# Kernel optimization log

Measured on AMD Instinct MI355X. Metric: run time of the kernel, lower is better.

The kernel has to match this reference:

```python
import jax, jax.numpy as jnp
import numpy as np

B, S, E, H, C = 2, 2048, 1024, 16, 16
SQ2 = np.float32(np.sqrt(2.0))


def setup_inputs() -> dict:
    key = jax.random.key(0)
    ks = jax.random.split(key, 32)
    sc = 0.02
    d = {"query": jax.random.normal(ks[0], (B, S, E), jnp.float32)}
    i = 1
    for dom in ("f", "w", "c"):
        d[f"Wp_{dom}"] = jax.random.normal(ks[i], (E, E), jnp.float32) * sc; i += 1
        d[f"bp_{dom}"] = jnp.zeros((E,), jnp.float32)
        d[f"Wc_{dom}"] = jax.random.normal(ks[i], (C, E, 3), jnp.float32) * sc; i += 1
        d[f"bc_{dom}"] = jnp.zeros((C,), jnp.float32)
        d["F" + dom] = jax.random.normal(ks[i], (C, E), jnp.float32); i += 1
    d["mha_iw"] = jax.random.normal(ks[i], (3 * E, E), jnp.float32) * sc; i += 1
    d["mha_ib"] = jnp.zeros((3 * E,), jnp.float32)
    d["mha_ow"] = jax.random.normal(ks[i], (E, E), jnp.float32) * sc; i += 1
    d["mha_ob"] = jnp.zeros((E,), jnp.float32)
    d["fus_W"] = jax.random.normal(ks[i], (E, 3 * E), jnp.float32) * sc; i += 1
    d["fus_b"] = jnp.zeros((E,), jnp.float32)
    return d


def _conv1d(x, W, b):
    # x: [B,S,E] real -> [B,S,C], conv over sequence, kernel 3, same padding
    y = jax.lax.conv_general_dilated(x.transpose(0, 2, 1), W, (1,), [(1, 1)],
                                     dimension_numbers=("NCH", "OIH", "NCH"))
    return (y + b[None, :, None]).transpose(0, 2, 1)


def _channels(x, Wc, bc, Fp):
    # spectral conv (real/imag separately if complex) + adaptive softmax filtering
    if jnp.iscomplexobj(x):
        ch = _conv1d(x.real, Wc, bc) + 1j * _conv1d(x.imag, Wc, bc)
    else:
        ch = _conv1d(x, Wc, bc)
    fw = jax.nn.softmax(Fp, axis=0)  # [C,E], softmax over channels
    return jnp.einsum("bsc,ce->bse", ch, fw.astype(ch.dtype))


def _spec_attn(q, k, v):
    scale = np.float32(1.0) / jnp.sqrt(jnp.asarray(q.shape[-1], jnp.float32))
    scores = jnp.einsum("bse,bte->bst", q, k) * scale
    if jnp.iscomplexobj(scores):
        w = jax.nn.softmax(scores.real, axis=-1)
        cw = (w * jnp.exp(1j * jnp.angle(scores))).astype(jnp.complex64)
        return jnp.einsum("bst,bte->bse", cw, v)
    return jnp.einsum("bst,bte->bse", jax.nn.softmax(scores, axis=-1), v)


def _haar(x):
    # simplified Haar wavelet transform; S is a power of 2 so no padding needed
    cur, coeffs = x, []
    while cur.shape[1] > 1:
        e, o = cur[:, 0::2, :], cur[:, 1::2, :]
        coeffs.append((e - o) / SQ2)
        cur = (e + o) / SQ2
    coeffs.append(cur)
    return jnp.concatenate(coeffs[::-1], axis=1)


def _dct_mats(L):
    n = jnp.arange(L, dtype=jnp.float32)
    k = n[:, None]
    D = jnp.cos(np.pi * k * (2.0 * n + 1.0) / (2.0 * L))
    D = D.at[0].multiply(np.float32(np.sqrt(1.0 / L)))
    D = D.at[1:].multiply(np.float32(np.sqrt(2.0 / L)))
    I = jnp.cos(np.pi * n * (2.0 * k + 1.0) / (2.0 * L))
    I = I.at[:, 0].multiply(np.float32(np.sqrt(1.0 / L)))
    I = I.at[:, 1:].multiply(np.float32(np.sqrt(2.0 / L)))
    return D, I


def _domain(x, Wp, bp, Wc, bc, Fp, domain):
    # key=value=query so q_domain == k_domain == v_domain
    xd = x @ Wp.T + bp
    if domain == "fourier":
        s = jnp.fft.fft(xd, axis=1)
        ch = _channels(s, Wc, bc, Fp)
        out = _spec_attn(ch, ch, ch)
        return jnp.fft.ifft(out, axis=1).real
    elif domain == "wavelet":
        s = _haar(xd)
        ch = _channels(s, Wc, bc, Fp)
        return _spec_attn(ch, ch, ch)  # inverse wavelet is identity in source
    else:  # cosine
        D, I = _dct_mats(xd.shape[1])
        s = jnp.einsum("st,bte->bse", D, xd)
        ch = _channels(s, Wc, bc, Fp)
        out = _spec_attn(ch, ch, ch)
        return jnp.einsum("st,bte->bse", I, out)


def _mha(x, iw, ib, ow, ob, nheads):
    # torch nn.MultiheadAttention (batch_first) self-attention
    Bx, L, Ex = x.shape
    hd = Ex // nheads
    qkv = x @ iw.T + ib
    q, k, v = jnp.split(qkv, 3, axis=-1)
    sh = lambda t: t.reshape(Bx, L, nheads, hd).transpose(0, 2, 1, 3)
    q, k, v = sh(q), sh(k), sh(v)
    a = jax.nn.softmax(jnp.einsum("bhld,bhmd->bhlm", q, k) / np.float32(np.sqrt(hd)), axis=-1)
    o = jnp.einsum("bhlm,bhmd->bhld", a, v).transpose(0, 2, 1, 3).reshape(Bx, L, Ex)
    return o @ ow.T + ob


def reference(query, Wp_f, bp_f, Wc_f, bc_f, Ff, Wp_w, bp_w, Wc_w, bc_w, Fw,
              Wp_c, bp_c, Wc_c, bc_c, Fc, mha_iw, mha_ib, mha_ow, mha_ob, fus_W, fus_b):
    outs = [
        _domain(query, Wp_f, bp_f, Wc_f, bc_f, Ff, "fourier"),
        _domain(query, Wp_w, bp_w, Wc_w, bc_w, Fw, "wavelet"),
        _domain(query, Wp_c, bp_c, Wc_c, bc_c, Fc, "cosine"),
    ]
    Bq, Sq, Eq = query.shape
    stacked = jnp.stack(outs, axis=2)                 # [B,S,3,E]
    corr = _mha(stacked.reshape(Bq * Sq, 3, Eq), mha_iw, mha_ib, mha_ow, mha_ob, H)
    fused = corr.reshape(Bq, Sq, 3 * Eq)              # concat of correlated domain outputs
    return fused @ fus_W.T + fus_b
```

## Files before the change

kernel.cpp:

```cpp
#include <hip/hip_runtime.h>
#include <cmath>

#define BB 2
#define SS_ 2048
#define EE 1024
#define CC 16

typedef __attribute__((ext_vector_type(8))) short short8v;
typedef __attribute__((ext_vector_type(4))) float floatx4;

#define BM 128
#define BN 128
#define BK 32
#define LDP 40

__device__ __forceinline__ void split4(const float4 v, short4& h, short4& l)
{
    unsigned ux = __float_as_uint(v.x), uy = __float_as_uint(v.y);
    unsigned uz = __float_as_uint(v.z), uw = __float_as_uint(v.w);
    h.x = (short)(ux >> 16); h.y = (short)(uy >> 16);
    h.z = (short)(uz >> 16); h.w = (short)(uw >> 16);
    float lx = v.x - __uint_as_float(ux & 0xFFFF0000u);
    float ly = v.y - __uint_as_float(uy & 0xFFFF0000u);
    float lz = v.z - __uint_as_float(uz & 0xFFFF0000u);
    float lw = v.w - __uint_as_float(uw & 0xFFFF0000u);
    l.x = (short)(__float_as_uint(lx) >> 16);
    l.y = (short)(__float_as_uint(ly) >> 16);
    l.z = (short)(__float_as_uint(lz) >> 16);
    l.w = (short)(__float_as_uint(lw) >> 16);
}

template<bool BETA, bool BIAS>
__launch_bounds__(256, 2)
__global__ void gemm_bf16x3(const float* __restrict__ A, const float* __restrict__ Bsrc,
                            float* __restrict__ C, const float* __restrict__ bias,
                            int K, int lda, int ldb, int ldc,
                            long sA, long sB, long sC, float alpha, float beta)
{
    __shared__ short sAh[BM * LDP], sAl[BM * LDP], sBh[BN * LDP], sBl[BN * LDP];
    const int bz = blockIdx.z;
    A += (size_t)bz * sA; Bsrc += (size_t)bz * sB; C += (size_t)bz * sC;
    const int tid = threadIdx.x;
    const int m0 = blockIdx.y * BM, n0 = blockIdx.x * BN;

    const int lr0 = tid >> 3;
    const int kc0 = (tid & 7) * 4;
    const float* pa = A + (size_t)(m0 + lr0) * lda + kc0;
    const float* pb = Bsrc + (size_t)(n0 + lr0) * ldb + kc0;

    float4 ra[4], rb[4];
    #pragma unroll
    for (int c = 0; c < 4; ++c) {
        ra[c] = *(const float4*)(pa + (size_t)c * 32 * lda);
        rb[c] = *(const float4*)(pb + (size_t)c * 32 * ldb);
    }

    const int lane = tid & 63, wid = tid >> 6;
    const int wm = wid >> 1, wn = wid & 1;
    const int lr = lane & 15, qd = lane >> 4;
    const int arow = wm * 64 + lr;
    const int brow = wn * 64 + lr;
    const int koff = qd * 8;

    floatx4 acc[4][4];
    #pragma unroll
    for (int i = 0; i < 4; ++i)
        #pragma unroll
        for (int j = 0; j < 4; ++j)
            acc[i][j] = (floatx4){0.f, 0.f, 0.f, 0.f};

    for (int kt = 0; kt < K; kt += BK) {
        __syncthreads();
        #pragma unroll
        for (int c = 0; c < 4; ++c) {
            const int row = lr0 + c * 32;
            short4 h, l;
            split4(ra[c], h, l);
            *(short4*)&sAh[row * LDP + kc0] = h;
            *(short4*)&sAl[row * LDP + kc0] = l;
            split4(rb[c], h, l);
            *(short4*)&sBh[row * LDP + kc0] = h;
            *(short4*)&sBl[row * LDP + kc0] = l;
        }
        __syncthreads();
        if (kt + BK < K) {
            pa += BK; pb += BK;
            #pragma unroll
            for (int c = 0; c < 4; ++c) {
                ra[c] = *(const float4*)(pa + (size_t)c * 32 * lda);
                rb[c] = *(const float4*)(pb + (size_t)c * 32 * ldb);
            }
        }
        short8v ah[4], al[4], bh[4], bl[4];
        #pragma unroll
        for (int i = 0; i < 4; ++i) {
            ah[i] = *(const short8v*)&sAh[(arow + i * 16) * LDP + koff];
            al[i] = *(const short8v*)&sAl[(arow + i * 16) * LDP + koff];
            bh[i] = *(const short8v*)&sBh[(brow + i * 16) * LDP + koff];
            bl[i] = *(const short8v*)&sBl[(brow + i * 16) * LDP + koff];
        }
        #pragma unroll
        for (int i = 0; i < 4; ++i)
            #pragma unroll
            for (int j = 0; j < 4; ++j)
                acc[i][j] = __builtin_amdgcn_mfma_f32_16x16x32_bf16(ah[i], bh[j], acc[i][j], 0, 0, 0);
        #pragma unroll
        for (int i = 0; i < 4; ++i)
            #pragma unroll
            for (int j = 0; j < 4; ++j)
                acc[i][j] = __builtin_amdgcn_mfma_f32_16x16x32_bf16(ah[i], bl[j], acc[i][j], 0, 0, 0);
        #pragma unroll
        for (int i = 0; i < 4; ++i)
            #pragma unroll
            for (int j = 0; j < 4; ++j)
                acc[i][j] = __builtin_amdgcn_mfma_f32_16x16x32_bf16(al[i], bh[j], acc[i][j], 0, 0, 0);
    }

    #pragma unroll
    for (int i = 0; i < 4; ++i) {
        const int mbase = m0 + wm * 64 + i * 16 + qd * 4;
        #pragma unroll
        for (int j = 0; j < 4; ++j) {
            const int n = n0 + wn * 64 + j * 16 + lr;
            float bv = 0.f;
            if (BIAS) bv = bias[n];
            #pragma unroll
            for (int r = 0; r < 4; ++r) {
                size_t off = (size_t)(mbase + r) * ldc + n;
                float v = alpha * acc[i][j][r];
                if (BETA) v += beta * C[off];
                if (BIAS) v += bv;
                C[off] = v;
            }
        }
    }
}

template<int NT, bool TA, bool TB, bool ATOMIC>
__launch_bounds__(256)
__global__ void skinny(const float* __restrict__ A, const float* __restrict__ Bs,
                       float* __restrict__ C,
                       int K, int lda, int ldb, int ldc,
                       long sA, long sB, long sC, float alpha, int KS)
{
    const int zb = blockIdx.z / KS, ks = blockIdx.z - zb * KS;
    A += (size_t)zb * sA; Bs += (size_t)zb * sB; C += (size_t)zb * sC;
    const int klen = K / KS;
    const int k0 = ks * klen;
    const int m0 = blockIdx.x * 64;
    __shared__ float sa[32][68];
    __shared__ float sb[32][(NT == 48) ? 52 : 20];
    const int tid = threadIdx.x;
    const int tm = tid >> 4, tn = tid & 15;
    constexpr int CN = NT / 16;
    float acc[4][CN] = {};

    for (int kc = k0; kc < k0 + klen; kc += 32) {
        __syncthreads();
        if (!TA) {
            #pragma unroll
            for (int cx = 0; cx < 2; ++cx) {
                int lin = cx * 256 + tid;
                int r = lin >> 3, c4 = (lin & 7) * 4;
                float4 v = *(const float4*)(A + (size_t)(m0 + r) * lda + kc + c4);
                sa[c4 + 0][r] = v.x; sa[c4 + 1][r] = v.y; sa[c4 + 2][r] = v.z; sa[c4 + 3][r] = v.w;
            }
        } else {
            #pragma unroll
            for (int cx = 0; cx < 2; ++cx) {
                int lin = cx * 256 + tid;
                int kk = lin >> 4, c4 = (lin & 15) * 4;
                *(float4*)&sa[kk][c4] = *(const float4*)(A + (size_t)(kc + kk) * lda + m0 + c4);
            }
        }
        if (!TB) {
            constexpr int NF4 = NT / 4;
            for (int lin = tid; lin < 32 * NF4; lin += 256) {
                int kk = lin / NF4, c4 = (lin % NF4) * 4;
                *(float4*)&sb[kk][c4] = *(const float4*)(Bs + (size_t)(kc + kk) * ldb + c4);
            }
        } else {
            for (int lin = tid; lin < 128; lin += 256) {
                int n = lin >> 3, c4 = (lin & 7) * 4;
                float4 v = *(const float4*)(Bs + (size_t)n * ldb + kc + c4);
                sb[c4 + 0][n] = v.x; sb[c4 + 1][n] = v.y; sb[c4 + 2][n] = v.z; sb[c4 + 3][n] = v.w;
            }
        }
        __syncthreads();
        #pragma unroll
        for (int kk = 0; kk < 32; ++kk) {
            float4 av = *(const float4*)&sa[kk][tm * 4];
            #pragma unroll
            for (int c = 0; c < CN; ++c) {
                float bv = sb[kk][tn * CN + c];
                acc[0][c] = fmaf(av.x, bv, acc[0][c]);
                acc[1][c] = fmaf(av.y, bv, acc[1][c]);
                acc[2][c] = fmaf(av.z, bv, acc[2][c]);
                acc[3][c] = fmaf(av.w, bv, acc[3][c]);
            }
        }
    }
    #pragma unroll
    for (int r = 0; r < 4; ++r)
        #pragma unroll
        for (int c = 0; c < CN; ++c) {
            int m = m0 + tm * 4 + r, n = tn * CN + c;
            float v = alpha * acc[r][c];
            if (ATOMIC) atomicAdd(&C[(size_t)m * ldc + n], v);
            else C[(size_t)m * ldc + n] = v;
        }
}

template<int NT, bool TA>
__launch_bounds__(256)
__global__ void skinny_multi(const float* __restrict__ A0, const float* __restrict__ A1,
                             const float* __restrict__ A2,
                             const float* __restrict__ B0, const float* __restrict__ B1,
                             const float* __restrict__ B2,
                             float* __restrict__ C0, float* __restrict__ C1,
                             float* __restrict__ C2,
                             int K, int lda, int ldb, int ldc,
                             long sB, long sC, float al0, float al1, float al2,
                             int nb, int KS)
{
    const int z = blockIdx.z;
    const int sel = z / (nb * KS);
    const int rem = z - sel * (nb * KS);
    const int zb = rem / KS, ks = rem - zb * KS;
    const float* A = sel == 0 ? A0 : (sel == 1 ? A1 : A2);
    const float* Bs = (sel == 0 ? B0 : (sel == 1 ? B1 : B2)) + (size_t)zb * sB;
    float* C = (sel == 0 ? C0 : (sel == 1 ? C1 : C2)) + (size_t)zb * sC;
    const float alpha = sel == 0 ? al0 : (sel == 1 ? al1 : al2);
    const int klen = K / KS;
    const int k0 = ks * klen;
    const int m0 = blockIdx.x * 64;
    __shared__ float sa[32][68];
    __shared__ float sb[32][(NT == 48) ? 52 : 20];
    const int tid = threadIdx.x;
    const int tm = tid >> 4, tn = tid & 15;
    constexpr int CN = NT / 16;
    float acc[4][CN] = {};

    for (int kc = k0; kc < k0 + klen; kc += 32) {
        __syncthreads();
        if (!TA) {
            #pragma unroll
            for (int cx = 0; cx < 2; ++cx) {
                int lin = cx * 256 + tid;
                int r = lin >> 3, c4 = (lin & 7) * 4;
                float4 v = *(const float4*)(A + (size_t)(m0 + r) * lda + kc + c4);
                sa[c4 + 0][r] = v.x; sa[c4 + 1][r] = v.y; sa[c4 + 2][r] = v.z; sa[c4 + 3][r] = v.w;
            }
        } else {
            #pragma unroll
            for (int cx = 0; cx < 2; ++cx) {
                int lin = cx * 256 + tid;
                int kk = lin >> 4, c4 = (lin & 15) * 4;
                *(float4*)&sa[kk][c4] = *(const float4*)(A + (size_t)(kc + kk) * lda + m0 + c4);
            }
        }
        {
            constexpr int NF4 = NT / 4;
            for (int lin = tid; lin < 32 * NF4; lin += 256) {
                int kk = lin / NF4, c4 = (lin % NF4) * 4;
                *(float4*)&sb[kk][c4] = *(const float4*)(Bs + (size_t)(kc + kk) * ldb + c4);
            }
        }
        __syncthreads();
        #pragma unroll
        for (int kk = 0; kk < 32; ++kk) {
            float4 av = *(const float4*)&sa[kk][tm * 4];
            #pragma unroll
            for (int c = 0; c < CN; ++c) {
                float bv = sb[kk][tn * CN + c];
                acc[0][c] = fmaf(av.x, bv, acc[0][c]);
                acc[1][c] = fmaf(av.y, bv, acc[1][c]);
                acc[2][c] = fmaf(av.z, bv, acc[2][c]);
                acc[3][c] = fmaf(av.w, bv, acc[3][c]);
            }
        }
    }
    #pragma unroll
    for (int r = 0; r < 4; ++r)
        #pragma unroll
        for (int c = 0; c < CN; ++c) {
            int m = m0 + tm * 4 + r, n = tn * CN + c;
            atomicAdd(&C[(size_t)m * ldc + n], alpha * acc[r][c]);
        }
}

__global__ void gen_trig(float* __restrict__ Cc, float* __restrict__ Sn,
                         float* __restrict__ D, float* __restrict__ I)
{
    size_t idx = (size_t)blockIdx.x * 256 + threadIdx.x;
    if (idx < 4194304) {
        int k = (int)(idx >> 11);
        int n = (int)(idx & 2047);
        int m = (k * n) & 2047;
        float ang = (float)(6.283185307179586 * (double)m / 2048.0);
        Cc[idx] = cosf(ang);
        Sn[idx] = -sinf(ang);
    } else {
        idx -= 4194304;
        int i = (int)(idx >> 11);
        int j = (int)(idx & 2047);
        const float r1 = 0.022097086912079608f;
        const float r2 = 0.03125f;
        const float pif = 3.14159265358979323846f;
        float a  = (pif * (float)i) * (float)(2 * j + 1) / 4096.0f;
        D[idx] = cosf(a) * (i == 0 ? r1 : r2);
        float ai = (pif * (float)j) * (float)(2 * i + 1) / 4096.0f;
        I[idx] = cosf(ai) * (j == 0 ? r1 : r2);
    }
}

__launch_bounds__(256)
__global__ void prep_fw_G(const float* __restrict__ F0, const float* __restrict__ F1,
                          const float* __restrict__ F2, float* __restrict__ fw,
                          float* __restrict__ G)
{
    const int d = blockIdx.x, tid = threadIdx.x;
    const float* Fp = d == 0 ? F0 : (d == 1 ? F1 : F2);
    __shared__ float sf[CC * 1028];
    #pragma unroll
    for (int k = 0; k < 4; ++k) {
        int e = tid + k * 256;
        float v[CC]; float m = -3.4e38f;
        #pragma unroll
        for (int c = 0; c < CC; ++c) { v[c] = Fp[c * EE + e]; m = fmaxf(m, v[c]); }
        float s = 0.f;
        #pragma unroll
        for (int c = 0; c < CC; ++c) { v[c] = expf(v[c] - m); s += v[c]; }
        float inv = 1.f / s;
        #pragma unroll
        for (int c = 0; c < CC; ++c) {
            float o = v[c] * inv;
            fw[d * CC * EE + c * EE + e] = o;
            sf[c * 1028 + e] = o;
        }
    }
    __syncthreads();
    const int a = tid >> 4, b = tid & 15;
    const float4* pa = (const float4*)&sf[a * 1028];
    const float4* pb = (const float4*)&sf[b * 1028];
    float s = 0.f;
    for (int i = 0; i < 256; ++i) {
        float4 x = pa[i], y = pb[i];
        s += x.x * y.x + x.y * y.y + x.z * y.z + x.w * y.w;
    }
    G[d * 256 + a * 16 + b] = s * 0.03125f;
}

__global__ void build_w2(const float* __restrict__ W0, const float* __restrict__ W1,
                         const float* __restrict__ W2_, float* __restrict__ W2cat)
{
    int idx = blockIdx.x * 256 + threadIdx.x;
    if (idx >= 3 * CC * EE * 3) return;
    int d = idx / 49152, r = idx % 49152;
    const float* Wc = d == 0 ? W0 : (d == 1 ? W1 : W2_);
    int c = r / 3072, e = (r % 3072) / 3, k = r % 3;
    W2cat[d * 49152 + e * 48 + c * 3 + k] = Wc[r];
}

__global__ void build_ub2(const float* __restrict__ b0, const float* __restrict__ b1,
                          const float* __restrict__ b2, const float* __restrict__ W2cat,
                          float* __restrict__ ub)
{
    const int d = blockIdx.x, tid = threadIdx.x;
    const float* bp = d == 0 ? b0 : (d == 1 ? b1 : b2);
    __shared__ float red[4][48];
    const int c = tid & 63, sl = tid >> 6;
    float s = 0.f;
    if (c < 48)
        for (int e = sl; e < EE; e += 4)
            s += bp[e] * W2cat[d * 49152 + e * 48 + c];
    if (c < 48) red[sl][c] = s;
    __syncthreads();
    if (tid < 48) ub[d * 48 + tid] = red[0][tid] + red[1][tid] + red[2][tid] + red[3][tid];
}

__global__ void init_bufs(float* __restrict__ base, const float* __restrict__ ub)
{
    size_t idx = (size_t)blockIdx.x * 256 + threadIdx.x;
    const size_t W3N = 147456, UN = 589824, ZN = 720896;
    if (idx >= W3N + UN + ZN) return;
    float v = 0.f;
    if (idx >= W3N && idx < W3N + UN) {
        size_t r = idx - W3N;
        int d = (int)(r / 196608), c = (int)(r % 48);
        v = ub[d * 48 + c];
    }
    base[idx] = v;
}

__global__ void ib_append(const float* __restrict__ ib, float* __restrict__ Pt)
{
    int idx = blockIdx.x * 256 + threadIdx.x;
    if (idx >= 9216) return;
    int d = idx / 3072, j = idx % 3072;
    Pt[d * 52224 + j * 17 + 16] = ib[j];
}

__launch_bounds__(256)
__global__ void build_M(const float* __restrict__ Pt, float* __restrict__ Mten)
{
    int blk = blockIdx.x;
    int h = blk / 9, lm = blk % 9;
    int l = lm / 3, m = lm % 3;
    __shared__ float sQ[64][17], sK[64][17];
    for (int lin = threadIdx.x; lin < 1088; lin += 256) {
        int d = lin / 17, a = lin % 17;
        sQ[d][a] = Pt[l * 52224 + (size_t)(h * 64 + d) * 17 + a];
        sK[d][a] = Pt[m * 52224 + (size_t)(1024 + h * 64 + d) * 17 + a];
    }
    __syncthreads();
    for (int o = threadIdx.x; o < 289; o += 256) {
        int a = o / 17, b = o % 17;
        float s = 0.f;
        for (int d = 0; d < 64; ++d) s += sQ[d][a] * sK[d][b];
        Mten[(size_t)blk * 289 + o] = 0.125f * s;
    }
}

__launch_bounds__(256)
__global__ void build_yb2(const float* __restrict__ ob, const float* __restrict__ fus_W,
                          const float* __restrict__ fus_b, float* __restrict__ yb)
{
    const int n = blockIdx.x * 4 + (threadIdx.x >> 6);
    const int lane = threadIdx.x & 63;
    float s = 0.f;
    for (int j = lane; j < 3072; j += 64)
        s += ob[j & 1023] * fus_W[(size_t)n * 3072 + j];
    #pragma unroll
    for (int off = 32; off > 0; off >>= 1) s += __shfl_xor(s, off, 64);
    if (lane == 0) yb[n] = s + fus_b[n];
}

__global__ void transpose_k(const float* __restrict__ X, float* __restrict__ XT,
                            int rows, int cols)
{
    __shared__ float tile[32][33];
    const int lx = threadIdx.x & 31, ly = threadIdx.x >> 5;
    const int r0 = blockIdx.y * 32, c0 = blockIdx.x * 32;
    #pragma unroll
    for (int p = 0; p < 4; ++p)
        tile[ly + p * 8][lx] = X[(size_t)(r0 + ly + p * 8) * cols + c0 + lx];
    __syncthreads();
    #pragma unroll
    for (int p = 0; p < 4; ++p)
        XT[(size_t)(c0 + ly + p * 8) * rows + r0 + lx] = tile[lx][ly + p * 8];
}

#define HCG 8
__launch_bounds__(256)
__global__ void haar_all(const float* __restrict__ U, float* __restrict__ T)
{
    __shared__ float A[2048 * HCG];
    __shared__ float Pp[1024 * HCG];
    const int g = blockIdx.x, b = blockIdx.y, tid = threadIdx.x;
    const float isq = 0.70710678118654752440f;
    for (int lin = tid; lin < 2048 * 2; lin += 256) {
        int r = lin >> 1, c4 = (lin & 1) * 4;
        *(float4*)&A[r * HCG + c4] =
            *(const float4*)(U + ((size_t)(b * 2048 + r)) * 48 + g * HCG + c4);
    }
    __syncthreads();
    float* cur = A; float* nxt = Pp;
    for (int h = 1024; h >= 1; h >>= 1) {
        for (int lin = tid; lin < h * HCG; lin += 256) {
            int i = lin >> 3, c = lin & 7;
            float e = cur[(2 * i) * HCG + c], o = cur[(2 * i + 1) * HCG + c];
            T[((size_t)(b * 2048 + h + i)) * 48 + g * HCG + c] = (e - o) * isq;
            nxt[i * HCG + c] = (e + o) * isq;
        }
        __syncthreads();
        float* t = cur; cur = nxt; nxt = t;
    }
    if (tid < HCG) T[((size_t)(b * 2048)) * 48 + g * HCG + tid] = cur[tid];
}

template<bool CPLX>
__launch_bounds__(256)
__global__ void conv_mix2(const float* __restrict__ Tre, const float* __restrict__ Tim,
                          const float* __restrict__ G, const float* __restrict__ bc,
                          float* __restrict__ chR, float* __restrict__ chI,
                          float* __restrict__ QR, float* __restrict__ QI)
{
    const int s0 = blockIdx.x * 64, b = blockIdx.y;
    const int tid = threadIdx.x;
    __shared__ float sR[66 * 49];
    __shared__ float sI[CPLX ? 66 * 49 : 1];
    __shared__ float scr[64 * 17];
    __shared__ float sci[CPLX ? 64 * 17 : 1];
    __shared__ float sG[256];
    if (tid < 256) sG[tid] = G[tid];
    for (int lin = tid; lin < 66 * 12; lin += 256) {
        int r = lin / 12, c4 = (lin % 12) * 4;
        int srow = s0 - 1 + r;
        float4 v = {0.f, 0.f, 0.f, 0.f}, w = {0.f, 0.f, 0.f, 0.f};
        if (srow >= 0 && srow < 2048) {
            v = *(const float4*)(Tre + ((size_t)(b * 2048 + srow)) * 48 + c4);
            if (CPLX) w = *(const float4*)(Tim + ((size_t)(b * 2048 + srow)) * 48 + c4);
        }
        sR[r * 49 + c4] = v.x; sR[r * 49 + c4 + 1] = v.y;
        sR[r * 49 + c4 + 2] = v.z; sR[r * 49 + c4 + 3] = v.w;
        if (CPLX) {
            sI[r * 49 + c4] = w.x; sI[r * 49 + c4 + 1] = w.y;
            sI[r * 49 + c4 + 2] = w.z; sI[r * 49 + c4 + 3] = w.w;
        }
    }
    __syncthreads();
    const int row = tid >> 2, ln = tid & 3;
    float ch[4], chi[4];
    #pragma unroll
    for (int j = 0; j < 4; ++j) {
        int c = ln * 4 + j;
        float bcv = bc[c];
        ch[j] = sR[row * 49 + 3 * c] + sR[(row + 1) * 49 + 3 * c + 1]
              + sR[(row + 2) * 49 + 3 * c + 2] + bcv;
        scr[row * 17 + c] = ch[j];
        if (CPLX) {
            chi[j] = sI[row * 49 + 3 * c] + sI[(row + 1) * 49 + 3 * c + 1]
                   + sI[(row + 2) * 49 + 3 * c + 2] + bcv;
            sci[row * 17 + c] = chi[j];
        }
    }
    size_t ro = ((size_t)(b * 2048 + s0 + row)) * 16 + ln * 4;
    *(float4*)(chR + ro) = *(float4*)&ch[0];
    if (CPLX) *(float4*)(chI + ro) = *(float4*)&chi[0];
    __syncthreads();
    float qp[4], qpi[4];
    #pragma unroll
    for (int j = 0; j < 4; ++j) { qp[j] = 0.f; qpi[j] = 0.f; }
    #pragma unroll
    for (int c = 0; c < 16; ++c) {
        float cv = scr[row * 17 + c];
        float cvi = CPLX ? sci[row * 17 + c] : 0.f;
        #pragma unroll
        for (int j = 0; j < 4; ++j) {
            float g = sG[c * 16 + ln * 4 + j];
            qp[j] = fmaf(cv, g, qp[j]);
            if (CPLX) qpi[j] = fmaf(cvi, g, qpi[j]);
        }
    }
    *(float4*)(QR + ro) = *(float4*)&qp[0];
    if (CPLX) *(float4*)(QI + ro) = *(float4*)&qpi[0];
}

__launch_bounds__(256)
__global__ void flash_r2(const float* __restrict__ Qp, const float* __restrict__ ch,
                         float* __restrict__ O)
{
    const int b = blockIdx.y;
    const int w = threadIdx.x >> 6, lane = threadIdx.x & 63;
    const int s = blockIdx.x * 4 + w;
    const float* qrow = Qp + ((size_t)(b * 2048 + s)) * 16;
    float q[16];
    #pragma unroll
    for (int j = 0; j < 4; ++j) *(float4*)&q[j * 4] = *(const float4*)(qrow + j * 4);
    const float* chb = ch + (size_t)b * 2048 * 16;
    float m = -3.4e38f, l = 0.f;
    float acc[16] = {};
    for (int t = lane; t < 2048; t += 64) {
        const float* kp = chb + (size_t)t * 16;
        float kv[16];
        #pragma unroll
        for (int j = 0; j < 4; ++j) *(float4*)&kv[j * 4] = *(const float4*)(kp + j * 4);
        float sc = 0.f;
        #pragma unroll
        for (int e = 0; e < 16; ++e) sc = fmaf(q[e], kv[e], sc);
        float mn = fmaxf(m, sc);
        float al = __expf(m - mn), p = __expf(sc - mn);
        l = l * al + p;
        #pragma unroll
        for (int e = 0; e < 16; ++e) acc[e] = fmaf(acc[e], al, p * kv[e]);
        m = mn;
    }
    #pragma unroll
    for (int off = 1; off < 64; off <<= 1) {
        float m2 = __shfl_xor(m, off, 64);
        float l2 = __shfl_xor(l, off, 64);
        float mn = fmaxf(m, m2);
        float ra = __expf(m - mn), rb = __expf(m2 - mn);
        l = l * ra + l2 * rb;
        #pragma unroll
        for (int e = 0; e < 16; ++e) {
            float a2 = __shfl_xor(acc[e], off, 64);
            acc[e] = acc[e] * ra + a2 * rb;
        }
        m = mn;
    }
    if (lane < 4) {
        float inv = 1.f / l;
        float4 o4 = {acc[lane * 4] * inv, acc[lane * 4 + 1] * inv,
                     acc[lane * 4 + 2] * inv, acc[lane * 4 + 3] * inv};
        *(float4*)(O + ((size_t)(b * 2048 + s)) * 16 + lane * 4) = o4;
    }
}

__launch_bounds__(256)
__global__ void flash_c2(const float* __restrict__ QpR, const float* __restrict__ QpI,
                         const float* __restrict__ chR, const float* __restrict__ chI,
                         float* __restrict__ OR_, float* __restrict__ OI_)
{
    const int b = blockIdx.y;
    const int w = threadIdx.x >> 6, lane = threadIdx.x & 63;
    const int s = blockIdx.x * 4 + w;
    float qr[16], qi[16];
    {
        const float* qrow = QpR + ((size_t)(b * 2048 + s)) * 16;
        const float* qrowI = QpI + ((size_t)(b * 2048 + s)) * 16;
        #pragma unroll
        for (int j = 0; j < 4; ++j) {
            *(float4*)&qr[j * 4] = *(const float4*)(qrow + j * 4);
            *(float4*)&qi[j * 4] = *(const float4*)(qrowI + j * 4);
        }
    }
    const float* cbR = chR + (size_t)b * 2048 * 16;
    const float* cbI = chI + (size_t)b * 2048 * 16;
    float m = -3.4e38f, l = 0.f;
    float aR[16] = {}, aI[16] = {};
    for (int t = lane; t < 2048; t += 64) {
        float kr[16], ki[16];
        #pragma unroll
        for (int j = 0; j < 4; ++j) {
            *(float4*)&kr[j * 4] = *(const float4*)(cbR + (size_t)t * 16 + j * 4);
            *(float4*)&ki[j * 4] = *(const float4*)(cbI + (size_t)t * 16 + j * 4);
        }
        float sre = 0.f, sim = 0.f;
        #pragma unroll
        for (int e = 0; e < 16; ++e) {
            sre = fmaf(qr[e], kr[e], sre); sre = fmaf(-qi[e], ki[e], sre);
            sim = fmaf(qr[e], ki[e], sim); sim = fmaf(qi[e], kr[e], sim);
        }
        float mn = fmaxf(m, sre);
        float al = __expf(m - mn), p = __expf(sre - mn);
        l = l * al + p;
        float rr = sqrtf(sre * sre + sim * sim);
        float iv = (rr > 0.f) ? (p / rr) : 0.f;
        float wr = (rr > 0.f) ? iv * sre : p;
        float wi = (rr > 0.f) ? iv * sim : 0.f;
        #pragma unroll
        for (int e = 0; e < 16; ++e) {
            aR[e] = fmaf(aR[e], al, wr * kr[e] - wi * ki[e]);
            aI[e] = fmaf(aI[e], al, wr * ki[e] + wi * kr[e]);
        }
        m = mn;
    }
    #pragma unroll
    for (int off = 1; off < 64; off <<= 1) {
        float m2 = __shfl_xor(m, off, 64);
        float l2 = __shfl_xor(l, off, 64);
        float mn = fmaxf(m, m2);
        float ra = __expf(m - mn), rb = __expf(m2 - mn);
        l = l * ra + l2 * rb;
        #pragma unroll
        for (int e = 0; e < 16; ++e) {
            float a2 = __shfl_xor(aR[e], off, 64);
            aR[e] = aR[e] * ra + a2 * rb;
            float b2 = __shfl_xor(aI[e], off, 64);
            aI[e] = aI[e] * ra + b2 * rb;
        }
        m = mn;
    }
    float inv = 1.f / l;
    size_t ro = ((size_t)(b * 2048 + s)) * 16;
    if (lane < 4) {
        float4 o4 = {aR[lane * 4] * inv, aR[lane * 4 + 1] * inv,
                     aR[lane * 4 + 2] * inv, aR[lane * 4 + 3] * inv};
        *(float4*)(OR_ + ro + lane * 4) = o4;
    } else if (lane < 8) {
        int j = lane - 4;
        float4 o4 = {aI[j * 4] * inv, aI[j * 4 + 1] * inv,
                     aI[j * 4 + 2] * inv, aI[j * 4 + 3] * inv};
        *(float4*)(OI_ + ro + j * 4) = o4;
    }
}

__launch_bounds__(256)
__global__ void mha_o(const float* __restrict__ R0, const float* __restrict__ R1,
                      const float* __restrict__ R2, const float* __restrict__ Pt,
                      const float* __restrict__ Mten, float* __restrict__ MO)
{
    const int tid = threadIdx.x;
    const int p = blockIdx.x * 256 + tid;
    const int h = blockIdx.y;
    __shared__ float sPv[3 * 64 * 20];
    __shared__ float sM[9 * 17 * 20];
    for (int lin = tid; lin < 3264; lin += 256) {
        int mm = lin / 1088, rem = lin % 1088;
        int rr = rem / 17, a = rem % 17;
        sPv[(mm * 64 + rr) * 20 + a] = Pt[mm * 52224 + (size_t)(2048 + h * 64 + rr) * 17 + a];
    }
    for (int lin = tid; lin < 2601; lin += 256) {
        int lm = lin / 289, rem = lin % 289;
        int a = rem / 17, bq = rem % 17;
        sM[lm * 340 + a * 20 + bq] = Mten[(size_t)h * 2601 + lin];
    }
    __syncthreads();
    float R[3][16];
    float4 R4[3][4];
    #pragma unroll
    for (int j = 0; j < 4; ++j) {
        R4[0][j] = *(const float4*)(R0 + (size_t)p * 16 + j * 4);
        R4[1][j] = *(const float4*)(R1 + (size_t)p * 16 + j * 4);
        R4[2][j] = *(const float4*)(R2 + (size_t)p * 16 + j * 4);
        *(float4*)&R[0][j * 4] = R4[0][j];
        *(float4*)&R[1][j * 4] = R4[1][j];
        *(float4*)&R[2][j * 4] = R4[2][j];
    }
    float w[3][3];
    #pragma unroll
    for (int l = 0; l < 3; ++l) {
        float sc[3];
        #pragma unroll
        for (int mm = 0; mm < 3; ++mm) {
            const float* Mp = &sM[(l * 3 + mm) * 340];
            float s = 0.f;
            #pragma unroll
            for (int a = 0; a < 17; ++a) {
                const float* mr = Mp + a * 20;
                float4 m0 = *(const float4*)(mr), m1 = *(const float4*)(mr + 4);
                float4 m2 = *(const float4*)(mr + 8), m3 = *(const float4*)(mr + 12);
                float t = mr[16];
                t = fmaf(m0.x, R4[mm][0].x, t); t = fmaf(m0.y, R4[mm][0].y, t);
                t = fmaf(m0.z, R4[mm][0].z, t); t = fmaf(m0.w, R4[mm][0].w, t);
                t = fmaf(m1.x, R4[mm][1].x, t); t = fmaf(m1.y, R4[mm][1].y, t);
                t = fmaf(m1.z, R4[mm][1].z, t); t = fmaf(m1.w, R4[mm][1].w, t);
                t = fmaf(m2.x, R4[mm][2].x, t); t = fmaf(m2.y, R4[mm][2].y, t);
                t = fmaf(m2.z, R4[mm][2].z, t); t = fmaf(m2.w, R4[mm][2].w, t);
                t = fmaf(m3.x, R4[mm][3].x, t); t = fmaf(m3.y, R4[mm][3].y, t);
                t = fmaf(m3.z, R4[mm][3].z, t); t = fmaf(m3.w, R4[mm][3].w, t);
                float ra = (a < 16) ? R[l][a] : 1.f;
                s = fmaf(ra, t, s);
            }
            sc[mm] = s;
        }
        float mx = fmaxf(sc[0], fmaxf(sc[1], sc[2]));
        float e0 = expf(sc[0] - mx), e1 = expf(sc[1] - mx), e2 = expf(sc[2] - mx);
        float inv = 1.f / (e0 + e1 + e2);
        w[l][0] = e0 * inv; w[l][1] = e1 * inv; w[l][2] = e2 * inv;
    }
    #pragma unroll
    for (int d4 = 0; d4 < 16; ++d4) {
        float4 vm[3];
        #pragma unroll
        for (int mm = 0; mm < 3; ++mm) {
            float vx[4];
            #pragma unroll
            for (int r = 0; r < 4; ++r) {
                const float* pv = &sPv[(mm * 64 + d4 * 4 + r) * 20];
                float4 p0 = *(const float4*)(pv), p1 = *(const float4*)(pv + 4);
                float4 p2 = *(const float4*)(pv + 8), p3 = *(const float4*)(pv + 12);
                float t = pv[16];
                t = fmaf(R4[mm][0].x, p0.x, t); t = fmaf(R4[mm][0].y, p0.y, t);
                t = fmaf(R4[mm][0].z, p0.z, t); t = fmaf(R4[mm][0].w, p0.w, t);
                t = fmaf(R4[mm][1].x, p1.x, t); t = fmaf(R4[mm][1].y, p1.y, t);
                t = fmaf(R4[mm][1].z, p1.z, t); t = fmaf(R4[mm][1].w, p1.w, t);
                t = fmaf(R4[mm][2].x, p2.x, t); t = fmaf(R4[mm][2].y, p2.y, t);
                t = fmaf(R4[mm][2].z, p2.z, t); t = fmaf(R4[mm][2].w, p2.w, t);
                t = fmaf(R4[mm][3].x, p3.x, t); t = fmaf(R4[mm][3].y, p3.y, t);
                t = fmaf(R4[mm][3].z, p3.z, t); t = fmaf(R4[mm][3].w, p3.w, t);
                vx[r] = t;
            }
            vm[mm] = (float4){vx[0], vx[1], vx[2], vx[3]};
        }
        #pragma unroll
        for (int l = 0; l < 3; ++l) {
            float4 o4;
            o4.x = w[l][0] * vm[0].x + w[l][1] * vm[1].x + w[l][2] * vm[2].x;
            o4.y = w[l][0] * vm[0].y + w[l][1] * vm[1].y + w[l][2] * vm[2].y;
            o4.z = w[l][0] * vm[0].z + w[l][1] * vm[1].z + w[l][2] * vm[2].z;
            o4.w = w[l][0] * vm[0].w + w[l][1] * vm[1].w + w[l][2] * vm[2].w;
            *(float4*)(MO + (size_t)p * 3072 + l * 1024 + h * 64 + d4 * 4) = o4;
        }
    }
}

static void gemm(hipStream_t st, const float* A, const float* Bsrc, float* C,
                 const float* bias, int M, int N, int K, int lda, int ldb, int ldc,
                 long sA, long sB, long sC, float alpha, float beta, int batch)
{
    dim3 g(N / BN, M / BM, batch), blk(256);
    bool ub = (beta != 0.0f), ubi = (bias != nullptr);
#define GCASE(BE, BI) gemm_bf16x3<BE, BI><<<g, blk, 0, st>>>(A, Bsrc, C, bias, K, lda, ldb, ldc, sA, sB, sC, alpha, beta)
    if (ub)  { if (ubi) GCASE(true, true);  else GCASE(true, false); }
    else     { if (ubi) GCASE(false, true); else GCASE(false, false); }
#undef GCASE
}

extern "C" void kernel_launch(void* const* d_in, const int* in_sizes, int n_in,
                              void* d_out, int out_size, void* d_ws, size_t ws_size,
                              hipStream_t stream)
{
    const float* query = (const float*)d_in[0];
    const float* Wp[3] = {(const float*)d_in[1], (const float*)d_in[6],  (const float*)d_in[11]};
    const float* bp[3] = {(const float*)d_in[2], (const float*)d_in[7],  (const float*)d_in[12]};
    const float* Wc[3] = {(const float*)d_in[3], (const float*)d_in[8],  (const float*)d_in[13]};
    const float* bc[3] = {(const float*)d_in[4], (const float*)d_in[9],  (const float*)d_in[14]};
    const float* Fp[3] = {(const float*)d_in[5], (const float*)d_in[10], (const float*)d_in[15]};
    const float* mha_iw = (const float*)d_in[16];
    const float* mha_ib = (const float*)d_in[17];
    const float* mha_ow = (const float*)d_in[18];
    const float* mha_ob = (const float*)d_in[19];
    const float* fus_W  = (const float*)d_in[20];
    const float* fus_b  = (const float*)d_in[21];
    float* out = (float*)d_out;
    float* ws = (float*)d_ws;

    size_t off = 0;
    auto alloc = [&](size_t n) { float* p = ws + off; off += n; return p; };
    float* MAT0 = alloc(4194304);
    float* MAT1 = alloc(4194304);
    float* DCTD = alloc(4194304);
    float* DCTI = alloc(4194304);
    float* MO   = alloc((size_t)4096 * 3072);
    float* FTb  = alloc((size_t)1024 * 3072);
    float* OWT  = alloc((size_t)1024 * 1024);
    float* fw   = alloc(3 * 16 * 1024);
    float* W2cat = alloc(147456);
    float* ubv  = alloc(256);
    float* Gm   = alloc(1024);
    float* W3cat = alloc(147456);
    float* Ucat = alloc(589824);
    float* Tfr  = alloc(196608);
    float* Tfi  = alloc(196608);
    float* Tc   = alloc(196608);
    float* Rf   = alloc(65536);
    float* Rc   = alloc(65536);
    float* Tw   = alloc(196608);
    float* chFr = alloc(65536); float* chFi = alloc(65536);
    float* QpFr = alloc(65536); float* QpFi = alloc(65536);
    float* chW  = alloc(65536); float* QpW  = alloc(65536);
    float* chC  = alloc(65536); float* QpC  = alloc(65536);
    float* OFr  = alloc(65536); float* OFi  = alloc(65536);
    float* Ow   = alloc(65536); float* Oc   = alloc(65536);
    float* Pt   = alloc(156672);
    float* Mten = alloc(41616);
    float* ybv  = alloc(1024);
    if (ws_size < off * sizeof(float)) return;

    float* Uf = Ucat, *Uw = Ucat + 196608, *Uc = Ucat + 2 * 196608;
    const long SE48 = 2048 * 48, SE16 = 2048 * 16;

    prep_fw_G<<<dim3(3), dim3(256), 0, stream>>>(Fp[0], Fp[1], Fp[2], fw, Gm);
    build_w2<<<dim3(576), dim3(256), 0, stream>>>(Wc[0], Wc[1], Wc[2], W2cat);
    build_ub2<<<dim3(3), dim3(256), 0, stream>>>(bp[0], bp[1], bp[2], W2cat, ubv);
    init_bufs<<<dim3((147456 + 589824 + 720896 + 255) / 256), dim3(256), 0, stream>>>(W3cat, ubv);
    gen_trig<<<dim3(32768), dim3(256), 0, stream>>>(MAT0, MAT1, DCTD, DCTI);

    skinny_multi<48, true><<<dim3(16, 1, 12), dim3(256), 0, stream>>>(
        Wp[0], Wp[1], Wp[2],
        W2cat, W2cat + 49152, W2cat + 2 * 49152,
        W3cat, W3cat + 49152, W3cat + 2 * 49152,
        1024, 1024, 48, 48, 0, 0, 1.f, 1.f, 1.f, 1, 4);

    skinny<48, false, false, true><<<dim3(64, 1, 6), dim3(256), 0, stream>>>(
        query, W3cat, Ucat, 1024, 1024, 48, 48, 0, 49152, 196608, 1.f, 2);

    skinny_multi<48, false><<<dim3(32, 1, 24), dim3(256), 0, stream>>>(
        MAT0, MAT1, DCTD, Uf, Uf, Uc, Tfr, Tfi, Tc,
        2048, 2048, 48, 48, SE48, SE48, 1.f, 1.f, 1.f, 2, 4);

    haar_all<<<dim3(6, 2), dim3(256), 0, stream>>>(Uw, Tw);

    conv_mix2<true><<<dim3(32, 2), dim3(256), 0, stream>>>(Tfr, Tfi, Gm, bc[0], chFr, chFi, QpFr, QpFi);
    conv_mix2<false><<<dim3(32, 2), dim3(256), 0, stream>>>(Tw, nullptr, Gm + 256, bc[1], chW, nullptr, QpW, nullptr);
    conv_mix2<false><<<dim3(32, 2), dim3(256), 0, stream>>>(Tc, nullptr, Gm + 512, bc[2], chC, nullptr, QpC, nullptr);

    flash_c2<<<dim3(512, 2), dim3(256), 0, stream>>>(QpFr, QpFi, chFr, chFi, OFr, OFi);
    flash_r2<<<dim3(512, 2), dim3(256), 0, stream>>>(QpW, chW, Ow);
    flash_r2<<<dim3(512, 2), dim3(256), 0, stream>>>(QpC, chC, Oc);

    skinny_multi<16, false><<<dim3(32, 1, 24), dim3(256), 0, stream>>>(
        MAT0, MAT1, DCTI, OFr, OFi, Oc, Rf, Rf, Rc,
        2048, 2048, 16, 16, SE16, SE16, 1.f / 2048.f, 1.f / 2048.f, 1.f, 2, 4);

    skinny<16, false, true, false><<<dim3(48, 1, 3), dim3(256), 0, stream>>>(
        mha_iw, fw, Pt, 1024, 1024, 1024, 17, 0, 16384, 52224, 1.f, 1);
    ib_append<<<dim3(36), dim3(256), 0, stream>>>(mha_ib, Pt);
    build_M<<<dim3(144), dim3(256), 0, stream>>>(Pt, Mten);

    mha_o<<<dim3(16, 16), dim3(256), 0, stream>>>(Rf, Ow, Rc, Pt, Mten, MO);

    transpose_k<<<dim3(32, 32), dim3(256), 0, stream>>>(mha_ow, OWT, 1024, 1024);
    gemm(stream, fus_W, OWT, FTb, nullptr, 1024, 1024, 1024, 3072, 1024, 3072,
         1024, 0, 1024, 1.f, 0.f, 3);
    build_yb2<<<dim3(256), dim3(256), 0, stream>>>(mha_ob, fus_W, fus_b, ybv);

    gemm(stream, MO, FTb, out, ybv, 4096, 1024, 3072, 3072, 3072, 1024,
         0, 0, 0, 1.f, 0.f, 1);
}
```

Measured before the change: 871.0 us.

## Move skinny GEMMs to bf16x3 MFMA and split-K large GEMMs with atomics

Replaces the scalar-FMA skinny GEMM kernels with an MFMA-based bf16x3 skinny kernel that can share operands across paired outputs. It also merges the conv and flash kernels into single multi-domain launches and adds split-K with atomic accumulation to the large fused GEMMs. Output, bias and accumulation buffers are now pre-initialised in one init kernel, and Wp is pre-transposed. The intent is to use the matrix cores for the skinny products and raise parallelism, at the cost of atomic traffic and extra zeroing and transposes.

```diff
diff --git a/kernel.cpp b/kernel.cpp
--- a/kernel.cpp
+++ b/kernel.cpp
@@ -8,11 +8,6 @@
 
 typedef __attribute__((ext_vector_type(8))) short short8v;
 typedef __attribute__((ext_vector_type(4))) float floatx4;
-
-#define BM 128
-#define BN 128
-#define BK 32
-#define LDP 40
 
 __device__ __forceinline__ void split4(const float4 v, short4& h, short4& l)
 {
@@ -30,23 +25,29 @@
     l.w = (short)(__float_as_uint(lw) >> 16);
 }
 
-template<bool BETA, bool BIAS>
+#define BM 128
+#define BN 128
+#define BK 32
+#define LDP 40
+
 __launch_bounds__(256, 2)
-__global__ void gemm_bf16x3(const float* __restrict__ A, const float* __restrict__ Bsrc,
-                            float* __restrict__ C, const float* __restrict__ bias,
-                            int K, int lda, int ldb, int ldc,
-                            long sA, long sB, long sC, float alpha, float beta)
+__global__ void gemm_at(const float* __restrict__ A, const float* __restrict__ Bsrc,
+                        float* __restrict__ C,
+                        int K, int lda, int ldb, int ldc,
+                        long sA, long sB, long sC, float alpha, int KS)
 {
     __shared__ short sAh[BM * LDP], sAl[BM * LDP], sBh[BN * LDP], sBl[BN * LDP];
-    const int bz = blockIdx.z;
+    const int z = blockIdx.z;
+    const int bz = z / KS, ks = z % KS;
+    const int klen = K / KS, kbase = ks * klen;
     A += (size_t)bz * sA; Bsrc += (size_t)bz * sB; C += (size_t)bz * sC;
     const int tid = threadIdx.x;
     const int m0 = blockIdx.y * BM, n0 = blockIdx.x * BN;
 
     const int lr0 = tid >> 3;
     const int kc0 = (tid & 7) * 4;
-    const float* pa = A + (size_t)(m0 + lr0) * lda + kc0;
-    const float* pb = Bsrc + (size_t)(n0 + lr0) * ldb + kc0;
+    const float* pa = A + (size_t)(m0 + lr0) * lda + kbase + kc0;
+    const float* pb = Bsrc + (size_t)(n0 + lr0) * ldb + kbase + kc0;
 
     float4 ra[4], rb[4];
     #pragma unroll
@@ -69,7 +70,7 @@
         for (int j = 0; j < 4; ++j)
             acc[i][j] = (floatx4){0.f, 0.f, 0.f, 0.f};
 
-    for (int kt = 0; kt < K; kt += BK) {
+    for (int kt = 0; kt < klen; kt += BK) {
         __syncthreads();
         #pragma unroll
         for (int c = 0; c < 4; ++c) {
@@ -83,7 +84,7 @@
             *(short4*)&sBl[row * LDP + kc0] = l;
         }
         __syncthreads();
-        if (kt + BK < K) {
+        if (kt + BK < klen) {
             pa += BK; pb += BK;
             #pragma unroll
             for (int c = 0; c < 4; ++c) {
@@ -122,170 +123,131 @@
         #pragma unroll
         for (int j = 0; j < 4; ++j) {
             const int n = n0 + wn * 64 + j * 16 + lr;
-            float bv = 0.f;
-            if (BIAS) bv = bias[n];
-            #pragma unroll
-            for (int r = 0; r < 4; ++r) {
-                size_t off = (size_t)(mbase + r) * ldc + n;
-                float v = alpha * acc[i][j][r];
-                if (BETA) v += beta * C[off];
-                if (BIAS) v += bv;
-                C[off] = v;
-            }
-        }
-    }
-}
-
-template<int NT, bool TA, bool TB, bool ATOMIC>
-__launch_bounds__(256)
-__global__ void skinny(const float* __restrict__ A, const float* __restrict__ Bs,
-                       float* __restrict__ C,
+            #pragma unroll
+            for (int r = 0; r < 4; ++r)
+                atomicAdd(&C[(size_t)(mbase + r) * ldc + n], alpha * acc[i][j][r]);
+        }
+    }
+}
+
+template<int NT, int MODE>
+__launch_bounds__(256, 4)
+__global__ void skmfma(const float* __restrict__ A0, const float* __restrict__ A1,
+                       const float* __restrict__ B0, const float* __restrict__ B1,
+                       float* __restrict__ C0, float* __restrict__ C1,
                        int K, int lda, int ldb, int ldc,
                        long sA, long sB, long sC, float alpha, int KS)
 {
-    const int zb = blockIdx.z / KS, ks = blockIdx.z - zb * KS;
-    A += (size_t)zb * sA; Bs += (size_t)zb * sB; C += (size_t)zb * sC;
-    const int klen = K / KS;
-    const int k0 = ks * klen;
+    constexpr int NA = (MODE >= 1) ? 2 : 1;
+    constexpr int NB = (MODE == 2) ? 2 : 1;
+    constexpr int NACC = (MODE == 1) ? 2 : 1;
+    constexpr int CT = NT / 16;
+    __shared__ short sAh[NA][64 * 40], sAl[NA][64 * 40];
+    __shared__ short sBh[NB][NT * 40], sBl[NB][NT * 40];
+    const int z = blockIdx.z;
+    const int zb = z / KS, ks = z % KS;
+    const int klen = K / KS, kbase = ks * klen;
+    const float* Ap[NA]; const float* Bp[NB]; float* Cp[NACC];
+    Ap[0] = A0 + (size_t)zb * sA;
+    if constexpr (NA == 2) Ap[1] = A1 + (size_t)zb * sA;
+    Bp[0] = B0 + (size_t)zb * sB;
+    if constexpr (NB == 2) Bp[1] = B1 + (size_t)zb * sB;
+    Cp[0] = C0 + (size_t)zb * sC;
+    if constexpr (NACC == 2) Cp[1] = C1 + (size_t)zb * sC;
+
+    const int tid = threadIdx.x;
     const int m0 = blockIdx.x * 64;
-    __shared__ float sa[32][68];
-    __shared__ float sb[32][(NT == 48) ? 52 : 20];
-    const int tid = threadIdx.x;
-    const int tm = tid >> 4, tn = tid & 15;
-    constexpr int CN = NT / 16;
-    float acc[4][CN] = {};
-
-    for (int kc = k0; kc < k0 + klen; kc += 32) {
+    const int arow = tid >> 2, akc = (tid & 3) * 8;
+    const int lane = tid & 63, w = tid >> 6;
+    const int lr = lane & 15, qd = lane >> 4;
+
+    floatx4 acc[NACC][CT];
+    #pragma unroll
+    for (int s = 0; s < NACC; ++s)
+        #pragma unroll
+        for (int j = 0; j < CT; ++j)
+            acc[s][j] = (floatx4){0.f, 0.f, 0.f, 0.f};
+
+    for (int kc = 0; kc < klen; kc += 32) {
         __syncthreads();
-        if (!TA) {
-            #pragma unroll
-            for (int cx = 0; cx < 2; ++cx) {
-                int lin = cx * 256 + tid;
-                int r = lin >> 3, c4 = (lin & 7) * 4;
-                float4 v = *(const float4*)(A + (size_t)(m0 + r) * lda + kc + c4);
-                sa[c4 + 0][r] = v.x; sa[c4 + 1][r] = v.y; sa[c4 + 2][r] = v.z; sa[c4 + 3][r] = v.w;
+        #pragma unroll
+        for (int s = 0; s < NA; ++s) {
+            const float* pa = Ap[s] + (size_t)(m0 + arow) * lda + kbase + kc + akc;
+            float4 v0 = *(const float4*)pa;
+            float4 v1 = *(const float4*)(pa + 4);
+            short4 h, l;
+            split4(v0, h, l);
+            *(short4*)&sAh[s][arow * 40 + akc] = h;
+            *(short4*)&sAl[s][arow * 40 + akc] = l;
+            split4(v1, h, l);
+            *(short4*)&sAh[s][arow * 40 + akc + 4] = h;
+            *(short4*)&sAl[s][arow * 40 + akc + 4] = l;
+        }
+        #pragma unroll
+        for (int s = 0; s < NB; ++s) {
+            for (int lin = tid; lin < 32 * (NT / 4); lin += 256) {
+                int kk = lin / (NT / 4), n4 = (lin % (NT / 4)) * 4;
+                float4 v = *(const float4*)(Bp[s] + (size_t)(kbase + kc + kk) * ldb + n4);
+                short4 h, l; split4(v, h, l);
+                sBh[s][(n4 + 0) * 40 + kk] = h.x; sBh[s][(n4 + 1) * 40 + kk] = h.y;
+                sBh[s][(n4 + 2) * 40 + kk] = h.z; sBh[s][(n4 + 3) * 40 + kk] = h.w;
+                sBl[s][(n4 + 0) * 40 + kk] = l.x; sBl[s][(n4 + 1) * 40 + kk] = l.y;
+                sBl[s][(n4 + 2) * 40 + kk] = l.z; sBl[s][(n4 + 3) * 40 + kk] = l.w;
+            }
+        }
+        __syncthreads();
+        short8v ah[NA], alv[NA];
+        #pragma unroll
+        for (int s = 0; s < NA; ++s) {
+            ah[s]  = *(const short8v*)&sAh[s][(w * 16 + lr) * 40 + qd * 8];
+            alv[s] = *(const short8v*)&sAl[s][(w * 16 + lr) * 40 + qd * 8];
+        }
+        short8v bh[NB][CT], bl[NB][CT];
+        #pragma unroll
+        for (int s = 0; s < NB; ++s)
+            #pragma unroll
+            for (int j = 0; j < CT; ++j) {
+                bh[s][j] = *(const short8v*)&sBh[s][(j * 16 + lr) * 40 + qd * 8];
+                bl[s][j] = *(const short8v*)&sBl[s][(j * 16 + lr) * 40 + qd * 8];
+            }
+        if constexpr (MODE == 0) {
+            #pragma unroll
+            for (int j = 0; j < CT; ++j) {
+                acc[0][j] = __builtin_amdgcn_mfma_f32_16x16x32_bf16(ah[0], bh[0][j], acc[0][j], 0, 0, 0);
+                acc[0][j] = __builtin_amdgcn_mfma_f32_16x16x32_bf16(ah[0], bl[0][j], acc[0][j], 0, 0, 0);
+                acc[0][j] = __builtin_amdgcn_mfma_f32_16x16x32_bf16(alv[0], bh[0][j], acc[0][j], 0, 0, 0);
+            }
+        } else if constexpr (MODE == 1) {
+            #pragma unroll
+            for (int j = 0; j < CT; ++j) {
+                acc[0][j] = __builtin_amdgcn_mfma_f32_16x16x32_bf16(ah[0], bh[0][j], acc[0][j], 0, 0, 0);
+                acc[0][j] = __builtin_amdgcn_mfma_f32_16x16x32_bf16(ah[0], bl[0][j], acc[0][j], 0, 0, 0);
+                acc[0][j] = __builtin_amdgcn_mfma_f32_16x16x32_bf16(alv[0], bh[0][j], acc[0][j], 0, 0, 0);
+                acc[1][j] = __builtin_amdgcn_mfma_f32_16x16x32_bf16(ah[1], bh[0][j], acc[1][j], 0, 0, 0);
+                acc[1][j] = __builtin_amdgcn_mfma_f32_16x16x32_bf16(ah[1], bl[0][j], acc[1][j], 0, 0, 0);
+                acc[1][j] = __builtin_amdgcn_mfma_f32_16x16x32_bf16(alv[1], bh[0][j], acc[1][j], 0, 0, 0);
             }
         } else {
             #pragma unroll
-            for (int cx = 0; cx < 2; ++cx) {
-                int lin = cx * 256 + tid;
-                int kk = lin >> 4, c4 = (lin & 15) * 4;
-                *(float4*)&sa[kk][c4] = *(const float4*)(A + (size_t)(kc + kk) * lda + m0 + c4);
+            for (int j = 0; j < CT; ++j) {
+                acc[0][j] = __builtin_amdgcn_mfma_f32_16x16x32_bf16(ah[0], bh[0][j], acc[0][j], 0, 0, 0);
+                acc[0][j] = __builtin_amdgcn_mfma_f32_16x16x32_bf16(ah[0], bl[0][j], acc[0][j], 0, 0, 0);
+                acc[0][j] = __builtin_amdgcn_mfma_f32_16x16x32_bf16(alv[0], bh[0][j], acc[0][j], 0, 0, 0);
+                acc[0][j] = __builtin_amdgcn_mfma_f32_16x16x32_bf16(ah[1], bh[1][j], acc[0][j], 0, 0, 0);
+                acc[0][j] = __builtin_amdgcn_mfma_f32_16x16x32_bf16(ah[1], bl[1][j], acc[0][j], 0, 0, 0);
+                acc[0][j] = __builtin_amdgcn_mfma_f32_16x16x32_bf16(alv[1], bh[1][j], acc[0][j], 0, 0, 0);
             }
         }
-        if (!TB) {
-            constexpr int NF4 = NT / 4;
-            for (int lin = tid; lin < 32 * NF4; lin += 256) {
-                int kk = lin / NF4, c4 = (lin % NF4) * 4;
-                *(float4*)&sb[kk][c4] = *(const float4*)(Bs + (size_t)(kc + kk) * ldb + c4);
-            }
-        } else {
-            for (int lin = tid; lin < 128; lin += 256) {
-                int n = lin >> 3, c4 = (lin & 7) * 4;
-                float4 v = *(const float4*)(Bs + (size_t)n * ldb + kc + c4);
-                sb[c4 + 0][n] = v.x; sb[c4 + 1][n] = v.y; sb[c4 + 2][n] = v.z; sb[c4 + 3][n] = v.w;
-            }
-        }
-        __syncthreads();
-        #pragma unroll
-        for (int kk = 0; kk < 32; ++kk) {
-            float4 av = *(const float4*)&sa[kk][tm * 4];
-            #pragma unroll
-            for (int c = 0; c < CN; ++c) {
-                float bv = sb[kk][tn * CN + c];
-                acc[0][c] = fmaf(av.x, bv, acc[0][c]);
-                acc[1][c] = fmaf(av.y, bv, acc[1][c]);
-                acc[2][c] = fmaf(av.z, bv, acc[2][c]);
-                acc[3][c] = fmaf(av.w, bv, acc[3][c]);
-            }
-        }
-    }
-    #pragma unroll
-    for (int r = 0; r < 4; ++r)
-        #pragma unroll
-        for (int c = 0; c < CN; ++c) {
-            int m = m0 + tm * 4 + r, n = tn * CN + c;
-            float v = alpha * acc[r][c];
-            if (ATOMIC) atomicAdd(&C[(size_t)m * ldc + n], v);
-            else C[(size_t)m * ldc + n] = v;
-        }
-}
-
-template<int NT, bool TA>
-__launch_bounds__(256)
-__global__ void skinny_multi(const float* __restrict__ A0, const float* __restrict__ A1,
-                             const float* __restrict__ A2,
-                             const float* __restrict__ B0, const float* __restrict__ B1,
-                             const float* __restrict__ B2,
-                             float* __restrict__ C0, float* __restrict__ C1,
-                             float* __restrict__ C2,
-                             int K, int lda, int ldb, int ldc,
-                             long sB, long sC, float al0, float al1, float al2,
-                             int nb, int KS)
-{
-    const int z = blockIdx.z;
-    const int sel = z / (nb * KS);
-    const int rem = z - sel * (nb * KS);
-    const int zb = rem / KS, ks = rem - zb * KS;
-    const float* A = sel == 0 ? A0 : (sel == 1 ? A1 : A2);
-    const float* Bs = (sel == 0 ? B0 : (sel == 1 ? B1 : B2)) + (size_t)zb * sB;
-    float* C = (sel == 0 ? C0 : (sel == 1 ? C1 : C2)) + (size_t)zb * sC;
-    const float alpha = sel == 0 ? al0 : (sel == 1 ? al1 : al2);
-    const int klen = K / KS;
-    const int k0 = ks * klen;
-    const int m0 = blockIdx.x * 64;
-    __shared__ float sa[32][68];
-    __shared__ float sb[32][(NT == 48) ? 52 : 20];
-    const int tid = threadIdx.x;
-    const int tm = tid >> 4, tn = tid & 15;
-    constexpr int CN = NT / 16;
-    float acc[4][CN] = {};
-
-    for (int kc = k0; kc < k0 + klen; kc += 32) {
-        __syncthreads();
-        if (!TA) {
-            #pragma unroll
-            for (int cx = 0; cx < 2; ++cx) {
-                int lin = cx * 256 + tid;
-                int r = lin >> 3, c4 = (lin & 7) * 4;
-                float4 v = *(const float4*)(A + (size_t)(m0 + r) * lda + kc + c4);
-                sa[c4 + 0][r] = v.x; sa[c4 + 1][r] = v.y; sa[c4 + 2][r] = v.z; sa[c4 + 3][r] = v.w;
-            }
-        } else {
-            #pragma unroll
-            for (int cx = 0; cx < 2; ++cx) {
-                int lin = cx * 256 + tid;
-                int kk = lin >> 4, c4 = (lin & 15) * 4;
-                *(float4*)&sa[kk][c4] = *(const float4*)(A + (size_t)(kc + kk) * lda + m0 + c4);
-            }
-        }
-        {
-            constexpr int NF4 = NT / 4;
-            for (int lin = tid; lin < 32 * NF4; lin += 256) {
-                int kk = lin / NF4, c4 = (lin % NF4) * 4;
-                *(float4*)&sb[kk][c4] = *(const float4*)(Bs + (size_t)(kc + kk) * ldb + c4);
-            }
-        }
-        __syncthreads();
-        #pragma unroll
-        for (int kk = 0; kk < 32; ++kk) {
-            float4 av = *(const float4*)&sa[kk][tm * 4];
-            #pragma unroll
-            for (int c = 0; c < CN; ++c) {
-                float bv = sb[kk][tn * CN + c];
-                acc[0][c] = fmaf(av.x, bv, acc[0][c]);
-                acc[1][c] = fmaf(av.y, bv, acc[1][c]);
-                acc[2][c] = fmaf(av.z, bv, acc[2][c]);
-                acc[3][c] = fmaf(av.w, bv, acc[3][c]);
-            }
-        }
-    }
-    #pragma unroll
-    for (int r = 0; r < 4; ++r)
-        #pragma unroll
-        for (int c = 0; c < CN; ++c) {
-            int m = m0 + tm * 4 + r, n = tn * CN + c;
-            atomicAdd(&C[(size_t)m * ldc + n], alpha * acc[r][c]);
+    }
+    #pragma unroll
+    for (int s = 0; s < NACC; ++s)
+        #pragma unroll
+        for (int j = 0; j < CT; ++j) {
+            const int n = j * 16 + lr;
+            const int mb = m0 + w * 16 + qd * 4;
+            #pragma unroll
+            for (int r = 0; r < 4; ++r)
+                atomicAdd(&Cp[s][(size_t)(mb + r) * ldc + n], alpha * acc[s][j][r]);
         }
 }
 
@@ -316,7 +278,7 @@
 
 __launch_bounds__(256)
 __global__ void prep_fw_G(const float* __restrict__ F0, const float* __restrict__ F1,
-                          const float* __restrict__ F2, float* __restrict__ fw,
+                          const float* __restrict__ F2, float* __restrict__ fwT,
                           float* __restrict__ G)
 {
     const int d = blockIdx.x, tid = threadIdx.x;
@@ -333,11 +295,10 @@
         for (int c = 0; c < CC; ++c) { v[c] = expf(v[c] - m); s += v[c]; }
         float inv = 1.f / s;
         #pragma unroll
-        for (int c = 0; c < CC; ++c) {
-            float o = v[c] * inv;
-            fw[d * CC * EE + c * EE + e] = o;
-            sf[c * 1028 + e] = o;
-        }
+        for (int c = 0; c < CC; ++c) { v[c] *= inv; sf[c * 1028 + e] = v[c]; }
+        #pragma unroll
+        for (int j = 0; j < 4; ++j)
+            *(float4*)(fwT + d * 16384 + (size_t)e * 16 + j * 4) = *(float4*)&v[j * 4];
     }
     __syncthreads();
     const int a = tid >> 4, b = tid & 15;
@@ -379,18 +340,44 @@
     if (tid < 48) ub[d * 48 + tid] = red[0][tid] + red[1][tid] + red[2][tid] + red[3][tid];
 }
 
-__global__ void init_bufs(float* __restrict__ base, const float* __restrict__ ub)
+__launch_bounds__(256)
+__global__ void build_yb2(const float* __restrict__ ob, const float* __restrict__ fus_W,
+                          const float* __restrict__ fus_b, float* __restrict__ yb)
+{
+    const int n = blockIdx.x * 4 + (threadIdx.x >> 6);
+    const int lane = threadIdx.x & 63;
+    float s = 0.f;
+    for (int j = lane; j < 3072; j += 64)
+        s += ob[j & 1023] * fus_W[(size_t)n * 3072 + j];
+    #pragma unroll
+    for (int off = 32; off > 0; off >>= 1) s += __shfl_xor(s, off, 64);
+    if (lane == 0) yb[n] = s + fus_b[n];
+}
+
+__global__ void init_all(float* __restrict__ zone1, const float* __restrict__ ub,
+                         float* __restrict__ Pt, float* __restrict__ FTb,
+                         float* __restrict__ out, const float* __restrict__ yb)
 {
     size_t idx = (size_t)blockIdx.x * 256 + threadIdx.x;
     const size_t W3N = 147456, UN = 589824, ZN = 720896;
-    if (idx >= W3N + UN + ZN) return;
-    float v = 0.f;
-    if (idx >= W3N && idx < W3N + UN) {
-        size_t r = idx - W3N;
-        int d = (int)(r / 196608), c = (int)(r % 48);
-        v = ub[d * 48 + c];
-    }
-    base[idx] = v;
+    const size_t Z1 = W3N + UN + ZN;
+    const size_t PTN = 156672, FTN = 3145728, ON = 4194304;
+    if (idx < Z1) {
+        float v = 0.f;
+        if (idx >= W3N && idx < W3N + UN) {
+            size_t r = idx - W3N;
+            int d = (int)(r / 196608), c = (int)(r % 48);
+            v = ub[d * 48 + c];
+        }
+        zone1[idx] = v;
+    } else if (idx < Z1 + PTN) {
+        Pt[idx - Z1] = 0.f;
+    } else if (idx < Z1 + PTN + FTN) {
+        FTb[idx - Z1 - PTN] = 0.f;
+    } else if (idx < Z1 + PTN + FTN + ON) {
+        size_t r = idx - Z1 - PTN - FTN;
+        out[r] = yb[r & 1023];
+    }
 }
 
 __global__ void ib_append(const float* __restrict__ ib, float* __restrict__ Pt)
@@ -422,20 +409,6 @@
     }
 }
 
-__launch_bounds__(256)
-__global__ void build_yb2(const float* __restrict__ ob, const float* __restrict__ fus_W,
-                          const float* __restrict__ fus_b, float* __restrict__ yb)
-{
-    const int n = blockIdx.x * 4 + (threadIdx.x >> 6);
-    const int lane = threadIdx.x & 63;
-    float s = 0.f;
-    for (int j = lane; j < 3072; j += 64)
-        s += ob[j & 1023] * fus_W[(size_t)n * 3072 + j];
-    #pragma unroll
-    for (int off = 32; off > 0; off >>= 1) s += __shfl_xor(s, off, 64);
-    if (lane == 0) yb[n] = s + fus_b[n];
-}
-
 __global__ void transpose_k(const float* __restrict__ X, float* __restrict__ XT,
                             int rows, int cols)
 {
@@ -451,7 +424,24 @@
         XT[(size_t)(c0 + ly + p * 8) * rows + r0 + lx] = tile[lx][ly + p * 8];
 }
 
-#define HCG 8
+__global__ void transpose_wp3(const float* __restrict__ W0, const float* __restrict__ W1,
+                              const float* __restrict__ W2, float* __restrict__ WT)
+{
+    __shared__ float tile[32][33];
+    const float* X = blockIdx.z == 0 ? W0 : (blockIdx.z == 1 ? W1 : W2);
+    float* T = WT + (size_t)blockIdx.z * 1048576;
+    const int lx = threadIdx.x & 31, ly = threadIdx.x >> 5;
+    const int r0 = blockIdx.y * 32, c0 = blockIdx.x * 32;
+    #pragma unroll
+    for (int p = 0; p < 4; ++p)
+        tile[ly + p * 8][lx] = X[(size_t)(r0 + ly + p * 8) * 1024 + c0 + lx];
+    __syncthreads();
+    #pragma unroll
+    for (int p = 0; p < 4; ++p)
+        T[(size_t)(c0 + ly + p * 8) * 1024 + r0 + lx] = tile[lx][ly + p * 8];
+}
+
+#define HCG 4
 __launch_bounds__(256)
 __global__ void haar_all(const float* __restrict__ U, float* __restrict__ T)
 {
@@ -459,16 +449,13 @@
     __shared__ float Pp[1024 * HCG];
     const int g = blockIdx.x, b = blockIdx.y, tid = threadIdx.x;
     const float isq = 0.70710678118654752440f;
-    for (int lin = tid; lin < 2048 * 2; lin += 256) {
-        int r = lin >> 1, c4 = (lin & 1) * 4;
-        *(float4*)&A[r * HCG + c4] =
-            *(const float4*)(U + ((size_t)(b * 2048 + r)) * 48 + g * HCG + c4);
-    }
+    for (int lin = tid; lin < 2048; lin += 256)
+        *(float4*)&A[lin * 4] = *(const float4*)(U + ((size_t)(b * 2048 + lin)) * 48 + g * HCG);
     __syncthreads();
     float* cur = A; float* nxt = Pp;
     for (int h = 1024; h >= 1; h >>= 1) {
         for (int lin = tid; lin < h * HCG; lin += 256) {
-            int i = lin >> 3, c = lin & 7;
+            int i = lin >> 2, c = lin & 3;
             float e = cur[(2 * i) * HCG + c], o = cur[(2 * i + 1) * HCG + c];
             T[((size_t)(b * 2048 + h + i)) * 48 + g * HCG + c] = (e - o) * isq;
             nxt[i * HCG + c] = (e + o) * isq;
@@ -479,19 +466,34 @@
     if (tid < HCG) T[((size_t)(b * 2048)) * 48 + g * HCG + tid] = cur[tid];
 }
 
-template<bool CPLX>
 __launch_bounds__(256)
-__global__ void conv_mix2(const float* __restrict__ Tre, const float* __restrict__ Tim,
-                          const float* __restrict__ G, const float* __restrict__ bc,
-                          float* __restrict__ chR, float* __restrict__ chI,
-                          float* __restrict__ QR, float* __restrict__ QI)
-{
+__global__ void conv_all(const float* __restrict__ Tfr, const float* __restrict__ Tfi,
+                         const float* __restrict__ Tw, const float* __restrict__ Tc,
+                         const float* __restrict__ Gm,
+                         const float* __restrict__ bc0, const float* __restrict__ bc1,
+                         const float* __restrict__ bc2,
+                         float* __restrict__ chFr, float* __restrict__ chFi,
+                         float* __restrict__ chW, float* __restrict__ chC,
+                         float* __restrict__ QFr, float* __restrict__ QFi,
+                         float* __restrict__ QW, float* __restrict__ QC)
+{
+    const int dom = blockIdx.z;
+    const bool cplx = (dom == 0);
+    const float* Tre = dom == 0 ? Tfr : (dom == 1 ? Tw : Tc);
+    const float* Tim = Tfi;
+    const float* G = Gm + dom * 256;
+    const float* bc = dom == 0 ? bc0 : (dom == 1 ? bc1 : bc2);
+    float* chR = dom == 0 ? chFr : (dom == 1 ? chW : chC);
+    float* chI = chFi;
+    float* QR = dom == 0 ? QFr : (dom == 1 ? QW : QC);
+    float* QI = QFi;
+
     const int s0 = blockIdx.x * 64, b = blockIdx.y;
     const int tid = threadIdx.x;
     __shared__ float sR[66 * 49];
-    __shared__ float sI[CPLX ? 66 * 49 : 1];
+    __shared__ float sI[66 * 49];
     __shared__ float scr[64 * 17];
-    __shared__ float sci[CPLX ? 64 * 17 : 1];
+    __shared__ float sci[64 * 17];
     __shared__ float sG[256];
     if (tid < 256) sG[tid] = G[tid];
     for (int lin = tid; lin < 66 * 12; lin += 256) {
@@ -500,11 +502,11 @@
         float4 v = {0.f, 0.f, 0.f, 0.f}, w = {0.f, 0.f, 0.f, 0.f};
         if (srow >= 0 && srow < 2048) {
             v = *(const float4*)(Tre + ((size_t)(b * 2048 + srow)) * 48 + c4);
-            if (CPLX) w = *(const float4*)(Tim + ((size_t)(b * 2048 + srow)) * 48 + c4);
+            if (cplx) w = *(const float4*)(Tim + ((size_t)(b * 2048 + srow)) * 48 + c4);
         }
         sR[r * 49 + c4] = v.x; sR[r * 49 + c4 + 1] = v.y;
         sR[r * 49 + c4 + 2] = v.z; sR[r * 49 + c4 + 3] = v.w;
-        if (CPLX) {
+        if (cplx) {
             sI[r * 49 + c4] = w.x; sI[r * 49 + c4 + 1] = w.y;
             sI[r * 49 + c4 + 2] = w.z; sI[r * 49 + c4 + 3] = w.w;
         }
@@ -519,7 +521,7 @@
         ch[j] = sR[row * 49 + 3 * c] + sR[(row + 1) * 49 + 3 * c + 1]
               + sR[(row + 2) * 49 + 3 * c + 2] + bcv;
         scr[row * 17 + c] = ch[j];
-        if (CPLX) {
+        if (cplx) {
             chi[j] = sI[row * 49 + 3 * c] + sI[(row + 1) * 49 + 3 * c + 1]
                    + sI[(row + 2) * 49 + 3 * c + 2] + bcv;
             sci[row * 17 + c] = chi[j];
@@ -527,97 +529,97 @@
     }
     size_t ro = ((size_t)(b * 2048 + s0 + row)) * 16 + ln * 4;
     *(float4*)(chR + ro) = *(float4*)&ch[0];
-    if (CPLX) *(float4*)(chI + ro) = *(float4*)&chi[0];
+    if (cplx) *(float4*)(chI + ro) = *(float4*)&chi[0];
     __syncthreads();
-    float qp[4], qpi[4];
-    #pragma unroll
-    for (int j = 0; j < 4; ++j) { qp[j] = 0.f; qpi[j] = 0.f; }
+    float qp[4] = {}, qpi[4] = {};
     #pragma unroll
     for (int c = 0; c < 16; ++c) {
         float cv = scr[row * 17 + c];
-        float cvi = CPLX ? sci[row * 17 + c] : 0.f;
+        float cvi = cplx ? sci[row * 17 + c] : 0.f;
         #pragma unroll
         for (int j = 0; j < 4; ++j) {
             float g = sG[c * 16 + ln * 4 + j];
             qp[j] = fmaf(cv, g, qp[j]);
-            if (CPLX) qpi[j] = fmaf(cvi, g, qpi[j]);
+            if (cplx) qpi[j] = fmaf(cvi, g, qpi[j]);
         }
     }
     *(float4*)(QR + ro) = *(float4*)&qp[0];
-    if (CPLX) *(float4*)(QI + ro) = *(float4*)&qpi[0];
+    if (cplx) *(float4*)(QI + ro) = *(float4*)&qpi[0];
 }
 
 __launch_bounds__(256)
-__global__ void flash_r2(const float* __restrict__ Qp, const float* __restrict__ ch,
-                         float* __restrict__ O)
-{
+__global__ void flash_all(const float* __restrict__ QpFr, const float* __restrict__ QpFi,
+                          const float* __restrict__ chFr, const float* __restrict__ chFi,
+                          float* __restrict__ OFr, float* __restrict__ OFi,
+                          const float* __restrict__ QpW, const float* __restrict__ chW,
+                          float* __restrict__ Ow_,
+                          const float* __restrict__ QpC, const float* __restrict__ chC,
+                          float* __restrict__ Oc_)
+{
+    const int dom = blockIdx.z;
     const int b = blockIdx.y;
     const int w = threadIdx.x >> 6, lane = threadIdx.x & 63;
     const int s = blockIdx.x * 4 + w;
-    const float* qrow = Qp + ((size_t)(b * 2048 + s)) * 16;
-    float q[16];
-    #pragma unroll
-    for (int j = 0; j < 4; ++j) *(float4*)&q[j * 4] = *(const float4*)(qrow + j * 4);
-    const float* chb = ch + (size_t)b * 2048 * 16;
-    float m = -3.4e38f, l = 0.f;
-    float acc[16] = {};
-    for (int t = lane; t < 2048; t += 64) {
-        const float* kp = chb + (size_t)t * 16;
-        float kv[16];
-        #pragma unroll
-        for (int j = 0; j < 4; ++j) *(float4*)&kv[j * 4] = *(const float4*)(kp + j * 4);
-        float sc = 0.f;
-        #pragma unroll
-        for (int e = 0; e < 16; ++e) sc = fmaf(q[e], kv[e], sc);
-        float mn = fmaxf(m, sc);
-        float al = __expf(m - mn), p = __expf(sc - mn);
-        l = l * al + p;
-        #pragma unroll
-        for (int e = 0; e < 16; ++e) acc[e] = fmaf(acc[e], al, p * kv[e]);
-        m = mn;
-    }
-    #pragma unroll
-    for (int off = 1; off < 64; off <<= 1) {
-        float m2 = __shfl_xor(m, off, 64);
-        float l2 = __shfl_xor(l, off, 64);
-        float mn = fmaxf(m, m2);
-        float ra = __expf(m - mn), rb = __expf(m2 - mn);
-        l = l * ra + l2 * rb;
-        #pragma unroll
-        for (int e = 0; e < 16; ++e) {
-            float a2 = __shfl_xor(acc[e], off, 64);
-            acc[e] = acc[e] * ra + a2 * rb;
-        }
-        m = mn;
-    }
-    if (lane < 4) {
-        float inv = 1.f / l;
-        float4 o4 = {acc[lane * 4] * inv, acc[lane * 4 + 1] * inv,
-                     acc[lane * 4 + 2] * inv, acc[lane * 4 + 3] * inv};
-        *(float4*)(O + ((size_t)(b * 2048 + s)) * 16 + lane * 4) = o4;
-    }
-}
-
-__launch_bounds__(256)
-__global__ void flash_c2(const float* __restrict__ QpR, const float* __restrict__ QpI,
-                         const float* __restrict__ chR, const float* __restrict__ chI,
-                         float* __restrict__ OR_, float* __restrict__ OI_)
-{
-    const int b = blockIdx.y;
-    const int w = threadIdx.x >> 6, lane = threadIdx.x & 63;
-    const int s = blockIdx.x * 4 + w;
+    if (dom != 0) {
+        const float* Qp = dom == 1 ? QpW : QpC;
+        const float* ch = dom == 1 ? chW : chC;
+        float* O = dom == 1 ? Ow_ : Oc_;
+        const float* qrow = Qp + ((size_t)(b * 2048 + s)) * 16;
+        float q[16];
+        #pragma unroll
+        for (int j = 0; j < 4; ++j) *(float4*)&q[j * 4] = *(const float4*)(qrow + j * 4);
+        const float* chb = ch + (size_t)b * 2048 * 16;
+        float m = -3.4e38f, l = 0.f;
+        float acc[16] = {};
+        for (int t = lane; t < 2048; t += 64) {
+            const float* kp = chb + (size_t)t * 16;
+            float kv[16];
+            #pragma unroll
+            for (int j = 0; j < 4; ++j) *(float4*)&kv[j * 4] = *(const float4*)(kp + j * 4);
+            float sc = 0.f;
+            #pragma unroll
+            for (int e = 0; e < 16; ++e) sc = fmaf(q[e], kv[e], sc);
+            float mn = fmaxf(m, sc);
+            float al = __expf(m - mn), p = __expf(sc - mn);
+            l = l * al + p;
+            #pragma unroll
+            for (int e = 0; e < 16; ++e) acc[e] = fmaf(acc[e], al, p * kv[e]);
+            m = mn;
+        }
+        #pragma unroll
+        for (int off = 1; off < 64; off <<= 1) {
+            float m2 = __shfl_xor(m, off, 64);
+            float l2 = __shfl_xor(l, off, 64);
+            float mn = fmaxf(m, m2);
+            float ra = __expf(m - mn), rb = __expf(m2 - mn);
+            l = l * ra + l2 * rb;
+            #pragma unroll
+            for (int e = 0; e < 16; ++e) {
+                float a2 = __shfl_xor(acc[e], off, 64);
+                acc[e] = acc[e] * ra + a2 * rb;
+            }
+            m = mn;
+        }
+        if (lane < 4) {
+            float inv = 1.f / l;
+            float4 o4 = {acc[lane * 4] * inv, acc[lane * 4 + 1] * inv,
+                         acc[lane * 4 + 2] * inv, acc[lane * 4 + 3] * inv};
+            *(float4*)(O + ((size_t)(b * 2048 + s)) * 16 + lane * 4) = o4;
+        }
+        return;
+    }
     float qr[16], qi[16];
     {
-        const float* qrow = QpR + ((size_t)(b * 2048 + s)) * 16;
-        const float* qrowI = QpI + ((size_t)(b * 2048 + s)) * 16;
+        const float* qrow = QpFr + ((size_t)(b * 2048 + s)) * 16;
+        const float* qrowI = QpFi + ((size_t)(b * 2048 + s)) * 16;
         #pragma unroll
         for (int j = 0; j < 4; ++j) {
             *(float4*)&qr[j * 4] = *(const float4*)(qrow + j * 4);
             *(float4*)&qi[j * 4] = *(const float4*)(qrowI + j * 4);
         }
     }
-    const float* cbR = chR + (size_t)b * 2048 * 16;
-    const float* cbI = chI + (size_t)b * 2048 * 16;
+    const float* cbR = chFr + (size_t)b * 2048 * 16;
+    const float* cbI = chFi + (size_t)b * 2048 * 16;
     float m = -3.4e38f, l = 0.f;
     float aR[16] = {}, aI[16] = {};
     for (int t = lane; t < 2048; t += 64) {
@@ -668,12 +670,12 @@
     if (lane < 4) {
         float4 o4 = {aR[lane * 4] * inv, aR[lane * 4 + 1] * inv,
                      aR[lane * 4 + 2] * inv, aR[lane * 4 + 3] * inv};
-        *(float4*)(OR_ + ro + lane * 4) = o4;
+        *(float4*)(OFr + ro + lane * 4) = o4;
     } else if (lane < 8) {
         int j = lane - 4;
         float4 o4 = {aI[j * 4] * inv, aI[j * 4 + 1] * inv,
                      aI[j * 4 + 2] * inv, aI[j * 4 + 3] * inv};
-        *(float4*)(OI_ + ro + j * 4) = o4;
+        *(float4*)(OFi + ro + j * 4) = o4;
     }
 }
 
@@ -777,18 +779,6 @@
     }
 }
 
-static void gemm(hipStream_t st, const float* A, const float* Bsrc, float* C,
-                 const float* bias, int M, int N, int K, int lda, int ldb, int ldc,
-                 long sA, long sB, long sC, float alpha, float beta, int batch)
-{
-    dim3 g(N / BN, M / BM, batch), blk(256);
-    bool ub = (beta != 0.0f), ubi = (bias != nullptr);
-#define GCASE(BE, BI) gemm_bf16x3<BE, BI><<<g, blk, 0, st>>>(A, Bsrc, C, bias, K, lda, ldb, ldc, sA, sB, sC, alpha, beta)
-    if (ub)  { if (ubi) GCASE(true, true);  else GCASE(true, false); }
-    else     { if (ubi) GCASE(false, true); else GCASE(false, false); }
-#undef GCASE
-}
-
 extern "C" void kernel_launch(void* const* d_in, const int* in_sizes, int n_in,
                               void* d_out, int out_size, void* d_ws, size_t ws_size,
                               hipStream_t stream)
@@ -817,7 +807,8 @@
     float* MO   = alloc((size_t)4096 * 3072);
     float* FTb  = alloc((size_t)1024 * 3072);
     float* OWT  = alloc((size_t)1024 * 1024);
-    float* fw   = alloc(3 * 16 * 1024);
+    float* WpT  = alloc(3145728);
+    float* fwT  = alloc(49152);
     float* W2cat = alloc(147456);
     float* ubv  = alloc(256);
     float* Gm   = alloc(1024);
@@ -843,51 +834,55 @@
     float* Uf = Ucat, *Uw = Ucat + 196608, *Uc = Ucat + 2 * 196608;
     const long SE48 = 2048 * 48, SE16 = 2048 * 16;
 
-    prep_fw_G<<<dim3(3), dim3(256), 0, stream>>>(Fp[0], Fp[1], Fp[2], fw, Gm);
     build_w2<<<dim3(576), dim3(256), 0, stream>>>(Wc[0], Wc[1], Wc[2], W2cat);
+    prep_fw_G<<<dim3(3), dim3(256), 0, stream>>>(Fp[0], Fp[1], Fp[2], fwT, Gm);
     build_ub2<<<dim3(3), dim3(256), 0, stream>>>(bp[0], bp[1], bp[2], W2cat, ubv);
-    init_bufs<<<dim3((147456 + 589824 + 720896 + 255) / 256), dim3(256), 0, stream>>>(W3cat, ubv);
+    build_yb2<<<dim3(256), dim3(256), 0, stream>>>(mha_ob, fus_W, fus_b, ybv);
     gen_trig<<<dim3(32768), dim3(256), 0, stream>>>(MAT0, MAT1, DCTD, DCTI);
-
-    skinny_multi<48, true><<<dim3(16, 1, 12), dim3(256), 0, stream>>>(
-        Wp[0], Wp[1], Wp[2],
-        W2cat, W2cat + 49152, W2cat + 2 * 49152,
-        W3cat, W3cat + 49152, W3cat + 2 * 49152,
-        1024, 1024, 48, 48, 0, 0, 1.f, 1.f, 1.f, 1, 4);
-
-    skinny<48, false, false, true><<<dim3(64, 1, 6), dim3(256), 0, stream>>>(
-        query, W3cat, Ucat, 1024, 1024, 48, 48, 0, 49152, 196608, 1.f, 2);
-
-    skinny_multi<48, false><<<dim3(32, 1, 24), dim3(256), 0, stream>>>(
-        MAT0, MAT1, DCTD, Uf, Uf, Uc, Tfr, Tfi, Tc,
-        2048, 2048, 48, 48, SE48, SE48, 1.f, 1.f, 1.f, 2, 4);
-
-    haar_all<<<dim3(6, 2), dim3(256), 0, stream>>>(Uw, Tw);
-
-    conv_mix2<true><<<dim3(32, 2), dim3(256), 0, stream>>>(Tfr, Tfi, Gm, bc[0], chFr, chFi, QpFr, QpFi);
-    conv_mix2<false><<<dim3(32, 2), dim3(256), 0, stream>>>(Tw, nullptr, Gm + 256, bc[1], chW, nullptr, QpW, nullptr);
-    conv_mix2<false><<<dim3(32, 2), dim3(256), 0, stream>>>(Tc, nullptr, Gm + 512, bc[2], chC, nullptr, QpC, nullptr);
-
-    flash_c2<<<dim3(512, 2), dim3(256), 0, stream>>>(QpFr, QpFi, chFr, chFi, OFr, OFi);
-    flash_r2<<<dim3(512, 2), dim3(256), 0, stream>>>(QpW, chW, Ow);
-    flash_r2<<<dim3(512, 2), dim3(256), 0, stream>>>(QpC, chC, Oc);
-
-    skinny_multi<16, false><<<dim3(32, 1, 24), dim3(256), 0, stream>>>(
-        MAT0, MAT1, DCTI, OFr, OFi, Oc, Rf, Rf, Rc,
-        2048, 2048, 16, 16, SE16, SE16, 1.f / 2048.f, 1.f / 2048.f, 1.f, 2, 4);
-
-    skinny<16, false, true, false><<<dim3(48, 1, 3), dim3(256), 0, stream>>>(
-        mha_iw, fw, Pt, 1024, 1024, 1024, 17, 0, 16384, 52224, 1.f, 1);
+    transpose_wp3<<<dim3(32, 32, 3), dim3(256), 0, stream>>>(Wp[0], Wp[1], Wp[2], WpT);
+    init_all<<<dim3(34980), dim3(256), 0, stream>>>(W3cat, ubv, Pt, FTb, out, ybv);
+
+    skmfma<48, 0><<<dim3(16, 1, 6), dim3(256), 0, stream>>>(
+        WpT, nullptr, W2cat, nullptr, W3cat, nullptr,
+        1024, 1024, 48, 48, 1048576, 49152, 49152, 1.f, 2);
+    skmfma<48, 0><<<dim3(64, 1, 6), dim3(256), 0, stream>>>(
+        query, nullptr, W3cat, nullptr, Ucat, nullptr,
+        1024, 1024, 48, 48, 0, 49152, 196608, 1.f, 2);
+    skmfma<48, 1><<<dim3(32, 1, 8), dim3(256), 0, stream>>>(
+        MAT0, MAT1, Uf, nullptr, Tfr, Tfi,
+        2048, 2048, 48, 48, 0, SE48, SE48, 1.f, 4);
+    skmfma<48, 0><<<dim3(32, 1, 8), dim3(256), 0, stream>>>(
+        DCTD, nullptr, Uc, nullptr, Tc, nullptr,
+        2048, 2048, 48, 48, 0, SE48, SE48, 1.f, 4);
+
+    haar_all<<<dim3(12, 2), dim3(256), 0, stream>>>(Uw, Tw);
+
+    conv_all<<<dim3(32, 2, 3), dim3(256), 0, stream>>>(
+        Tfr, Tfi, Tw, Tc, Gm, bc[0], bc[1], bc[2],
+        chFr, chFi, chW, chC, QpFr, QpFi, QpW, QpC);
+
+    flash_all<<<dim3(512, 2, 3), dim3(256), 0, stream>>>(
+        QpFr, QpFi, chFr, chFi, OFr, OFi, QpW, chW, Ow, QpC, chC, Oc);
+
+    skmfma<16, 2><<<dim3(32, 1, 8), dim3(256), 0, stream>>>(
+        MAT0, MAT1, OFr, OFi, Rf, nullptr,
+        2048, 2048, 16, 16, 0, SE16, SE16, 1.f / 2048.f, 4);
+    skmfma<16, 0><<<dim3(32, 1, 8), dim3(256), 0, stream>>>(
+        DCTI, nullptr, Oc, nullptr, Rc, nullptr,
+        2048, 2048, 16, 16, 0, SE16, SE16, 1.f, 4);
+    skmfma<16, 0><<<dim3(48, 1, 6), dim3(256), 0, stream>>>(
+        mha_iw, nullptr, fwT, nullptr, Pt, nullptr,
+        1024, 1024, 16, 17, 0, 16384, 52224, 1.f, 2);
+
     ib_append<<<dim3(36), dim3(256), 0, stream>>>(mha_ib, Pt);
     build_M<<<dim3(144), dim3(256), 0, stream>>>(Pt, Mten);
 
     mha_o<<<dim3(16, 16), dim3(256), 0, stream>>>(Rf, Ow, Rc, Pt, Mten, MO);
 
     transpose_k<<<dim3(32, 32), dim3(256), 0, stream>>>(mha_ow, OWT, 1024, 1024);
-    gemm(stream, fus_W, OWT, FTb, nullptr, 1024, 1024, 1024, 3072, 1024, 3072,
-         1024, 0, 1024, 1.f, 0.f, 3);
-    build_yb2<<<dim3(256), dim3(256), 0, stream>>>(mha_ob, fus_W, fus_b, ybv);
-
-    gemm(stream, MO, FTb, out, ybv, 4096, 1024, 3072, 3072, 3072, 1024,
-         0, 0, 0, 1.f, 0.f, 1);
-}
+    gemm_at<<<dim3(8, 8, 6), dim3(256), 0, stream>>>(
+        fus_W, OWT, FTb, 1024, 3072, 1024, 3072, 1024, 0, 1024, 1.f, 2);
+
+    gemm_at<<<dim3(8, 32, 2), dim3(256), 0, stream>>>(
+        MO, FTb, out, 3072, 3072, 3072, 1024, 0, 0, 0, 1.f, 2);
+}
```

Measured after the change: 765.7 us. -12.1%, faster.
